# Kernel optimization log

Hardware: AMD Instinct MI355X
Metric: run time of the kernel (lower is better)

## Reference

```python
import jax, jax.numpy as jnp
import numpy as np
import math

D = 768
H = 12
DFF = 3072
HD = D // H


def _layernorm(x, g, b, eps=1e-5):
    mu = jnp.mean(x, axis=-1, keepdims=True)
    var = jnp.var(x, axis=-1, keepdims=True)
    return (x - mu) * jax.lax.rsqrt(var + eps) * g + b


def setup_inputs() -> dict:
    key = jax.random.key(0)
    ks = jax.random.split(key, 12)
    B, S = 2, 4096
    s = 1.0 / math.sqrt(D)
    sf = 1.0 / math.sqrt(DFF)
    return {
        "x": jax.random.normal(ks[0], (B, S, D), jnp.float32),
        "attention_mask": jnp.ones((B, S), jnp.int32),
        "ln1_g": jnp.ones((D,), jnp.float32),
        "ln1_b": jnp.zeros((D,), jnp.float32),
        "ln2_g": jnp.ones((D,), jnp.float32),
        "ln2_b": jnp.zeros((D,), jnp.float32),
        "Wq": jax.random.normal(ks[1], (D, D), jnp.float32) * s,
        "bq": jnp.zeros((D,), jnp.float32),
        "Wk": jax.random.normal(ks[2], (D, D), jnp.float32) * s,
        "bk": jnp.zeros((D,), jnp.float32),
        "Wv": jax.random.normal(ks[3], (D, D), jnp.float32) * s,
        "bv": jnp.zeros((D,), jnp.float32),
        "Wo": jax.random.normal(ks[4], (D, D), jnp.float32) * s,
        "bo": jnp.zeros((D,), jnp.float32),
        "W1": jax.random.normal(ks[5], (D, DFF), jnp.float32) * s,
        "b1": jnp.zeros((DFF,), jnp.float32),
        "W2": jax.random.normal(ks[6], (DFF, D), jnp.float32) * sf,
        "b2": jnp.zeros((D,), jnp.float32),
    }


def _block(x, attention_mask, ln1_g, ln1_b, ln2_g, ln2_b,
           Wq, bq, Wk, bk, Wv, bv, Wo, bo, W1, b1, W2, b2):
    B, S, _ = x.shape
    h = _layernorm(x, ln1_g, ln1_b)
    q = (h @ Wq + bq).reshape(B, S, H, HD)
    k = (h @ Wk + bk).reshape(B, S, H, HD)
    v = (h @ Wv + bv).reshape(B, S, H, HD)
    # scores: [B, H, S, S]
    dots = jnp.einsum('bqhd,bkhd->bhqk', q, k) / math.sqrt(HD)
    causal = jnp.tril(jnp.ones((S, S), bool))  # True = keep
    keep = causal[None, None] & (attention_mask != 0)[:, None, None, :]
    dots = jnp.where(keep, dots, -jnp.inf)
    probs = jax.nn.softmax(dots, axis=-1)
    ctx = jnp.einsum('bhqk,bkhd->bqhd', probs, v).reshape(B, S, D)
    sa = ctx @ Wo + bo  # dropout = identity (eval)
    x = x + sa
    h2 = _layernorm(x, ln2_g, ln2_b)
    ff = jax.nn.relu(h2 @ W1 + b1) @ W2 + b2
    return x + ff


def reference(x, attention_mask, ln1_g, ln1_b, ln2_g, ln2_b,
              Wq, bq, Wk, bk, Wv, bv, Wo, bo, W1, b1, W2, b2):
    return _block(x, attention_mask, ln1_g, ln1_b, ln2_g, ln2_b,
                  Wq, bq, Wk, bk, Wv, bv, Wo, bo, W1, b1, W2, b2)
```

## Files before the change

### kernel.cpp

```cpp
#include <hip/hip_runtime.h>
#include <hip/hip_bf16.h>
#include <math.h>

#define S_LEN 4096
#define DMODEL 768
#define NHEAD 12
#define HDIM 64
#define DFF_ 3072
#define MROWS 8192

typedef __bf16 bf16;
typedef __bf16 bf16x4 __attribute__((ext_vector_type(4)));
typedef __bf16 bf16x8 __attribute__((ext_vector_type(8)));
typedef float f32x4 __attribute__((ext_vector_type(4)));
typedef short s16x4 __attribute__((ext_vector_type(4)));

union F4 { float4 v; float f[4]; };
union U2 { bf16 h[2]; unsigned u; };
union U8 { unsigned u[4]; bf16x8 v; };

#if __has_builtin(__builtin_amdgcn_mfma_f32_16x16x16bf16_1k)
typedef s16x4 mf16_t;
#define MFMA16(a, b, c) __builtin_amdgcn_mfma_f32_16x16x16bf16_1k((a), (b), (c), 0, 0, 0)
#define HAVE_MFMA16 1
#elif __has_builtin(__builtin_amdgcn_mfma_f32_16x16x16_bf16)
typedef bf16x4 mf16_t;
#define MFMA16(a, b, c) __builtin_amdgcn_mfma_f32_16x16x16_bf16((a), (b), (c), 0, 0, 0)
#define HAVE_MFMA16 1
#else
#define HAVE_MFMA16 0
#endif

#if HAVE_MFMA16
union U4 { unsigned u[2]; mf16_t v; };
#endif

__device__ __forceinline__ void gld_lds16(void* lds, const void* g) {
    __builtin_amdgcn_global_load_lds(
        (const __attribute__((address_space(1))) unsigned int*)g,
        (__attribute__((address_space(3))) unsigned int*)lds, 16, 0, 0);
}

template<typename OUT>
__global__ __launch_bounds__(256) void ln_kernel(const float* __restrict__ x,
                                                 const float* __restrict__ g,
                                                 const float* __restrict__ bta,
                                                 OUT* __restrict__ out,
                                                 float* __restrict__ zb) {
    const int row = blockIdx.x;
    const int t = threadIdx.x;
    if (zb && row == 0 && t < 192)
        ((float4*)zb)[t] = make_float4(0.f, 0.f, 0.f, 0.f);
    const float* xr = x + (size_t)row * DMODEL;
    float v0 = xr[t], v1 = xr[t + 256], v2 = xr[t + 512];
    float s = v0 + v1 + v2;
    float ss = v0 * v0 + v1 * v1 + v2 * v2;
    for (int o = 32; o > 0; o >>= 1) {
        s += __shfl_down(s, o, 64);
        ss += __shfl_down(ss, o, 64);
    }
    __shared__ float sm[4], sm2[4];
    const int w = t >> 6, lane = t & 63;
    if (lane == 0) { sm[w] = s; sm2[w] = ss; }
    __syncthreads();
    s = sm[0] + sm[1] + sm[2] + sm[3];
    ss = sm2[0] + sm2[1] + sm2[2] + sm2[3];
    const float mu = s * (1.0f / DMODEL);
    const float var = ss * (1.0f / DMODEL) - mu * mu;
    const float rs = rsqrtf(var + 1e-5f);
    OUT* orow = out + (size_t)row * DMODEL;
    orow[t]       = (OUT)((v0 - mu) * rs * g[t]       + bta[t]);
    orow[t + 256] = (OUT)((v1 - mu) * rs * g[t + 256] + bta[t + 256]);
    orow[t + 512] = (OUT)((v2 - mu) * rs * g[t + 512] + bta[t + 512]);
}

__global__ __launch_bounds__(256) void wtrans_all_kernel(
    const float* __restrict__ Wq, const float* __restrict__ Wk,
    const float* __restrict__ Wv, const float* __restrict__ Wo,
    const float* __restrict__ W1, const float* __restrict__ W2,
    bf16* __restrict__ Wqt, bf16* __restrict__ Wkt, bf16* __restrict__ Wvt,
    bf16* __restrict__ Wot, bf16* __restrict__ W1t, bf16* __restrict__ W2t) {
    int t = blockIdx.x;
    const float* W; bf16* Wt; int K, N;
    if      (t < 144)  { W = Wq; Wt = Wqt; K = 768;  N = 768;  }
    else if (t < 288)  { W = Wk; Wt = Wkt; K = 768;  N = 768;  t -= 144; }
    else if (t < 432)  { W = Wv; Wt = Wvt; K = 768;  N = 768;  t -= 288; }
    else if (t < 576)  { W = Wo; Wt = Wot; K = 768;  N = 768;  t -= 432; }
    else if (t < 1152) { W = W1; Wt = W1t; K = 768;  N = 3072; t -= 576; }
    else               { W = W2; Wt = W2t; K = 3072; N = 768;  t -= 1152; }
    const int nx = N >> 6;
    const int n0 = (t % nx) * 64, k0 = (t / nx) * 64;

    __shared__ float tile[64][65];
    const int tid = threadIdx.x;
    const int lr = tid >> 4, lc = (tid & 15) << 2;
#pragma unroll
    for (int i = 0; i < 4; ++i) {
        const int r = lr + i * 16;
        F4 w; w.v = *(const float4*)&W[(size_t)(k0 + r) * N + n0 + lc];
#pragma unroll
        for (int j = 0; j < 4; ++j) tile[r][lc + j] = w.f[j];
    }
    __syncthreads();
#pragma unroll
    for (int i = 0; i < 4; ++i) {
        const int n = lr + i * 16;
        bf16x4 o;
#pragma unroll
        for (int j = 0; j < 4; ++j) o[j] = (bf16)tile[lc + j][n];
        *(bf16x4*)&Wt[(size_t)(n0 + n) * K + k0 + lc] = o;
    }
}

template<int MT, bool RELU, bool RES, bool OUT_BF16>
__global__ __launch_bounds__(256) void mgemm_kernel(
    const bf16* __restrict__ A,
    const bf16* __restrict__ Wt0, const float* __restrict__ bias0, void* __restrict__ C0,
    const bf16* __restrict__ Wt1, const float* __restrict__ bias1, void* __restrict__ C1,
    const bf16* __restrict__ Wt2, const float* __restrict__ bias2, void* __restrict__ C2,
    const float* __restrict__ R, int M, int N, int K, int Kloop,
    int koff0, int koff1, int koff2,
    float sc0, float sc1, float sc2) {
    const bf16* Wt = Wt0; const float* bias = bias0; void* C = C0; float sc = sc0; int koff = koff0;
    if (blockIdx.z == 1) { Wt = Wt1; bias = bias1; C = C1; sc = sc1; koff = koff1; }
    if (blockIdx.z == 2) { Wt = Wt2; bias = bias2; C = C2; sc = sc2; koff = koff2; }

    const int gx = gridDim.x;
    const int nwg = gx * gridDim.y;
    const int chunk = nwg >> 3;
    int lid = blockIdx.y * gx + blockIdx.x;
    lid = (lid & 7) * chunk + (lid >> 3);
    const int row0 = (lid / gx) * MT, col0 = (lid % gx) * 128;

    constexpr int NI = (MT == 128) ? 4 : 2;
    __shared__ bf16 As[2][MT * 32];
    __shared__ bf16 Bs[2][128 * 32];

    const int tid = threadIdx.x;
    const int wave = tid >> 6, lane = tid & 63;
    const int wr = (MT == 128) ? (wave >> 1) * 64 : 0;
    const int wc = (MT == 128) ? (wave & 1) * 64 : wave * 32;
    const int mrow = lane & 15, kq = (lane >> 4) * 8;

    const int st_row = (lane >> 2);
    const int st_off = (lane & 3) * 16;

    f32x4 acc[4][NI] = {};

    const char* Ab = (const char*)(A + (size_t)row0 * K + koff);
    const char* Bb = (const char*)(Wt + (size_t)col0 * K + koff);
    const size_t strideA = (size_t)K * 2;

    for (int k0 = 0; k0 < Kloop; k0 += 64) {
#pragma unroll
        for (int s = 0; s < 2; ++s) {
            const int kk = k0 + s * 32;
            if (MT == 128) {
#pragma unroll
                for (int issue = 0; issue < 2; ++issue) {
                    const int r = wave * 32 + issue * 16 + st_row;
                    gld_lds16((char*)As[s] + (wave * 32 + issue * 16) * 64,
                              Ab + (size_t)r * strideA + kk * 2 + st_off);
                }
            } else {
                const int r = wave * 16 + st_row;
                gld_lds16((char*)As[s] + (wave * 16) * 64,
                          Ab + (size_t)r * strideA + kk * 2 + st_off);
            }
#pragma unroll
            for (int issue = 0; issue < 2; ++issue) {
                const int r = wave * 32 + issue * 16 + st_row;
                gld_lds16((char*)Bs[s] + (wave * 32 + issue * 16) * 64,
                          Bb + (size_t)r * strideA + kk * 2 + st_off);
            }
        }
        __syncthreads();
#pragma unroll
        for (int s = 0; s < 2; ++s) {
            bf16x8 af[4], bfr[NI];
#pragma unroll
            for (int mi = 0; mi < 4; ++mi)
                af[mi] = *(const bf16x8*)&As[s][(wr + mi * 16 + mrow) * 32 + kq];
#pragma unroll
            for (int ni = 0; ni < NI; ++ni)
                bfr[ni] = *(const bf16x8*)&Bs[s][(wc + ni * 16 + mrow) * 32 + kq];
#pragma unroll
            for (int mi = 0; mi < 4; ++mi)
#pragma unroll
                for (int ni = 0; ni < NI; ++ni)
                    acc[mi][ni] = __builtin_amdgcn_mfma_f32_16x16x32_bf16(
                        bfr[ni], af[mi], acc[mi][ni], 0, 0, 0);
        }
        __syncthreads();
    }

    const int quad = lane >> 4;
#pragma unroll
    for (int ni = 0; ni < NI; ++ni) {
        const int col = col0 + wc + ni * 16 + quad * 4;
        F4 bv4; bv4.v = *(const float4*)&bias[col];
#pragma unroll
        for (int mi = 0; mi < 4; ++mi) {
            const int row = row0 + wr + mi * 16 + mrow;
            F4 o;
#pragma unroll
            for (int r = 0; r < 4; ++r) o.f[r] = acc[mi][ni][r] + bv4.f[r];
            if (RES) {
                F4 rr; rr.v = *(const float4*)&R[(size_t)row * N + col];
#pragma unroll
                for (int r = 0; r < 4; ++r) o.f[r] += rr.f[r];
            }
#pragma unroll
            for (int r = 0; r < 4; ++r) {
                o.f[r] *= sc;
                if (RELU) o.f[r] = fmaxf(o.f[r], 0.0f);
            }
            if (OUT_BF16) {
                bf16x4 ob;
#pragma unroll
                for (int r = 0; r < 4; ++r) ob[r] = (bf16)o.f[r];
                *(bf16x4*)&((bf16*)C)[(size_t)row * N + col] = ob;
            } else {
                *(float4*)&((float*)C)[(size_t)row * N + col] = o.v;
            }
        }
    }
}

__global__ __launch_bounds__(256) void mattn_kernel(
    const bf16* __restrict__ Q, const bf16* __restrict__ K,
    const bf16* __restrict__ V, const int* __restrict__ amask,
    bf16* __restrict__ O) {
    const int bx = blockIdx.x, h = blockIdx.y, b = blockIdx.z;

    __shared__ bf16 Ks[2][64][68];
#if HAVE_MFMA16
    __shared__ bf16 Vt[2][80][68];
#else
    __shared__ bf16 Vt[2][64][68];
#endif
    __shared__ bf16 Os[64][68];
    __shared__ float mk[2][64];
    __shared__ int flagv[2];

    const int tid = threadIdx.x;
    const int wave = tid >> 6, lane = tid & 63;
    const int l = lane & 15, quad = lane >> 4;
#if !HAVE_MFMA16
    const int qh = quad >> 1;
    const int srcA = (quad & 1) * 32 + l;
    const int srcB = srcA + 16;
#endif
    const float NEG_INF = -__builtin_huge_valf();

    const int kr = tid >> 2, ks = (tid & 3) * 16;
    const int vk0 = (tid & 31) * 2, vds = (tid >> 5) * 8;

    const bf16* Kbase = K + (size_t)b * S_LEN * DMODEL + h * HDIM;
    const bf16* Vbase = V + (size_t)b * S_LEN * DMODEL + h * HDIM;

#if HAVE_MFMA16
    if (tid < 68) {
        Vt[0][64][tid] = (bf16)1.0f;
        Vt[1][64][tid] = (bf16)1.0f;
    }
#endif

#pragma unroll 1
    for (int pass = 0; pass < 2; ++pass) {
        const int qt = pass ? bx : (63 - bx);

        const bf16* Qb = Q + (size_t)(b * S_LEN + qt * 64 + wave * 16 + l) * DMODEL + h * HDIM;
        const bf16x8 qf0 = *(const bf16x8*)(Qb + quad * 8);
        const bf16x8 qf1 = *(const bf16x8*)(Qb + 32 + quad * 8);

        float m_run = NEG_INF;
#if !HAVE_MFMA16
        float l_run = 0.0f;
#endif
        f32x4 acc[4] = {};
#if HAVE_MFMA16
        f32x4 acc_l = {};
#endif

        bf16x8 kp0, kp1, vp0, vp1;
        int mv = 1;
        {
            const bf16* kg = Kbase + (size_t)kr * DMODEL + ks;
            kp0 = *(const bf16x8*)kg;
            kp1 = *(const bf16x8*)(kg + 8);
            const bf16* vg = Vbase + (size_t)vk0 * DMODEL + vds;
            vp0 = *(const bf16x8*)vg;
            vp1 = *(const bf16x8*)(vg + DMODEL);
            if (wave == 0) mv = amask[b * S_LEN + lane];
        }
        __syncthreads();
        {
            *(bf16x8*)&Ks[0][kr][ks]     = kp0;
            *(bf16x8*)&Ks[0][kr][ks + 8] = kp1;
#pragma unroll
            for (int i = 0; i < 8; ++i) {
                U2 w; w.h[0] = vp0[i]; w.h[1] = vp1[i];
                *(unsigned*)&Vt[0][vds + i][vk0] = w.u;
            }
            if (wave == 0) {
                mk[0][lane] = mv ? 0.0f : NEG_INF;
                unsigned long long bal = __ballot(mv != 0);
                if (lane == 0) flagv[0] = (bal == ~0ULL);
            }
        }
        __syncthreads();
        int buf = 0;

        for (int kt = 0; kt <= qt; ++kt) {
            const bool more = (kt < qt);
            if (more) {
                const bf16* kg = Kbase + (size_t)((kt + 1) * 64 + kr) * DMODEL + ks;
                kp0 = *(const bf16x8*)kg;
                kp1 = *(const bf16x8*)(kg + 8);
                const bf16* vg = Vbase + (size_t)((kt + 1) * 64 + vk0) * DMODEL + vds;
                vp0 = *(const bf16x8*)vg;
                vp1 = *(const bf16x8*)(vg + DMODEL);
                if (wave == 0) mv = amask[b * S_LEN + (kt + 1) * 64 + lane];
            }

            const int allv = flagv[buf];
            f32x4 sreg[4] = {};
            __builtin_amdgcn_s_setprio(1);
#pragma unroll
            for (int mi = 0; mi < 4; ++mi) {
                bf16x8 kf0 = *(const bf16x8*)&Ks[buf][mi * 16 + l][quad * 8];
                bf16x8 kf1 = *(const bf16x8*)&Ks[buf][mi * 16 + l][32 + quad * 8];
                sreg[mi] = __builtin_amdgcn_mfma_f32_16x16x32_bf16(kf0, qf0, sreg[mi], 0, 0, 0);
                sreg[mi] = __builtin_amdgcn_mfma_f32_16x16x32_bf16(kf1, qf1, sreg[mi], 0, 0, 0);
            }
            __builtin_amdgcn_s_setprio(0);
            if (!allv) {
#pragma unroll
                for (int mi = 0; mi < 4; ++mi) {
                    F4 m4; m4.v = *(const float4*)&mk[buf][mi * 16 + quad * 4];
#pragma unroll
                    for (int r = 0; r < 4; ++r) sreg[mi][r] += m4.f[r];
                }
            }
            if (kt == qt) {
#pragma unroll
                for (int mi = 0; mi < 4; ++mi)
#pragma unroll
                    for (int r = 0; r < 4; ++r)
                        if (mi * 16 + quad * 4 + r > wave * 16 + l)
                            sreg[mi][r] = NEG_INF;
            }

            float mloc = sreg[0][0];
#pragma unroll
            for (int mi = 0; mi < 4; ++mi)
#pragma unroll
                for (int r = 0; r < 4; ++r) mloc = fmaxf(mloc, sreg[mi][r]);
            mloc = fmaxf(mloc, __shfl_xor(mloc, 16, 64));
            mloc = fmaxf(mloc, __shfl_xor(mloc, 32, 64));
            if (__any(mloc > m_run + 8.0f)) {
                const float mn = fmaxf(m_run, mloc);
                const float alpha = __builtin_amdgcn_exp2f(m_run - mn);
                m_run = mn;
#pragma unroll
                for (int mi = 0; mi < 4; ++mi)
#pragma unroll
                    for (int r = 0; r < 4; ++r) acc[mi][r] *= alpha;
#if HAVE_MFMA16
#pragma unroll
                for (int r = 0; r < 4; ++r) acc_l[r] *= alpha;
#else
                l_run *= alpha;
#endif
            }
#pragma unroll
            for (int mi = 0; mi < 4; ++mi)
#pragma unroll
                for (int r = 0; r < 4; ++r)
                    sreg[mi][r] = __builtin_amdgcn_exp2f(sreg[mi][r] - m_run);
#if !HAVE_MFMA16
            float ls = 0.0f;
#pragma unroll
            for (int mi = 0; mi < 4; ++mi)
#pragma unroll
                for (int r = 0; r < 4; ++r) ls += sreg[mi][r];
            ls += __shfl_xor(ls, 16, 64);
            ls += __shfl_xor(ls, 32, 64);
            l_run += ls;
#endif

            unsigned pk[4][2];
#pragma unroll
            for (int mi = 0; mi < 4; ++mi) {
                U2 w0; w0.h[0] = (bf16)sreg[mi][0]; w0.h[1] = (bf16)sreg[mi][1];
                U2 w1; w1.h[0] = (bf16)sreg[mi][2]; w1.h[1] = (bf16)sreg[mi][3];
                pk[mi][0] = w0.u; pk[mi][1] = w1.u;
            }

#if HAVE_MFMA16
            __builtin_amdgcn_s_setprio(1);
#pragma unroll
            for (int mi = 0; mi < 4; ++mi) {
                U4 pb; pb.u[0] = pk[mi][0]; pb.u[1] = pk[mi][1];
#pragma unroll
                for (int di = 0; di < 4; ++di) {
                    mf16_t va = *(const mf16_t*)&Vt[buf][di * 16 + l][mi * 16 + quad * 4];
                    acc[di] = MFMA16(va, pb.v, acc[di]);
                }
                mf16_t vl = *(const mf16_t*)&Vt[buf][64 + l][mi * 16 + quad * 4];
                acc_l = MFMA16(vl, pb.v, acc_l);
            }
            __builtin_amdgcn_s_setprio(0);
#else
            bf16x8 pfrag[2];
#pragma unroll
            for (int kc = 0; kc < 2; ++kc) {
                U8 u;
#pragma unroll
                for (int t = 0; t < 2; ++t) {
                    const unsigned a0 = (unsigned)__shfl((int)pk[2 * kc][t],     srcA, 64);
                    const unsigned b0 = (unsigned)__shfl((int)pk[2 * kc + 1][t], srcA, 64);
                    u.u[t] = qh ? b0 : a0;
                    const unsigned a1 = (unsigned)__shfl((int)pk[2 * kc][t],     srcB, 64);
                    const unsigned b1 = (unsigned)__shfl((int)pk[2 * kc + 1][t], srcB, 64);
                    u.u[2 + t] = qh ? b1 : a1;
                }
                pfrag[kc] = u.v;
            }
#pragma unroll
            for (int mi = 0; mi < 4; ++mi) {
                bf16x8 vf0 = *(const bf16x8*)&Vt[buf][mi * 16 + l][quad * 8];
                bf16x8 vf1 = *(const bf16x8*)&Vt[buf][mi * 16 + l][32 + quad * 8];
                acc[mi] = __builtin_amdgcn_mfma_f32_16x16x32_bf16(vf0, pfrag[0], acc[mi], 0, 0, 0);
                acc[mi] = __builtin_amdgcn_mfma_f32_16x16x32_bf16(vf1, pfrag[1], acc[mi], 0, 0, 0);
            }
#endif

            if (more) {
                const int nb = buf ^ 1;
                *(bf16x8*)&Ks[nb][kr][ks]     = kp0;
                *(bf16x8*)&Ks[nb][kr][ks + 8] = kp1;
#pragma unroll
                for (int i = 0; i < 8; ++i) {
                    U2 w; w.h[0] = vp0[i]; w.h[1] = vp1[i];
                    *(unsigned*)&Vt[nb][vds + i][vk0] = w.u;
                }
                if (wave == 0) {
                    mk[nb][lane] = mv ? 0.0f : NEG_INF;
                    unsigned long long bal = __ballot(mv != 0);
                    if (lane == 0) flagv[nb] = (bal == ~0ULL);
                }
            }
            __syncthreads();
            buf ^= 1;
        }

#if HAVE_MFMA16
        const float l_run = __shfl(acc_l[0], l, 64);
#endif
        const float rinv = 1.0f / l_run;
#pragma unroll
        for (int mi = 0; mi < 4; ++mi) {
            U2 w0; w0.h[0] = (bf16)(acc[mi][0] * rinv); w0.h[1] = (bf16)(acc[mi][1] * rinv);
            U2 w1; w1.h[0] = (bf16)(acc[mi][2] * rinv); w1.h[1] = (bf16)(acc[mi][3] * rinv);
            *(unsigned*)&Os[wave * 16 + l][mi * 16 + quad * 4]     = w0.u;
            *(unsigned*)&Os[wave * 16 + l][mi * 16 + quad * 4 + 2] = w1.u;
        }
        __syncthreads();
        {
            const int orow = tid >> 2, oseg = (tid & 3) * 16;
            bf16* Og = O + (size_t)(b * S_LEN + qt * 64 + orow) * DMODEL + h * HDIM + oseg;
            *(bf16x8*)Og       = *(const bf16x8*)&Os[orow][oseg];
            *(bf16x8*)(Og + 8) = *(const bf16x8*)&Os[orow][oseg + 8];
        }
    }
}

extern "C" void kernel_launch(void* const* d_in, const int* in_sizes, int n_in,
                              void* d_out, int out_size, void* d_ws, size_t ws_size,
                              hipStream_t stream) {
    const float* x     = (const float*)d_in[0];
    const int*   amask = (const int*)  d_in[1];
    const float* ln1_g = (const float*)d_in[2];
    const float* ln1_b = (const float*)d_in[3];
    const float* ln2_g = (const float*)d_in[4];
    const float* ln2_b = (const float*)d_in[5];
    const float* Wq = (const float*)d_in[6];  const float* bq = (const float*)d_in[7];
    const float* Wk = (const float*)d_in[8];  const float* bk = (const float*)d_in[9];
    const float* Wv = (const float*)d_in[10]; const float* bv = (const float*)d_in[11];
    const float* Wo = (const float*)d_in[12]; const float* bo = (const float*)d_in[13];
    const float* W1 = (const float*)d_in[14]; const float* b1 = (const float*)d_in[15];
    const float* W2 = (const float*)d_in[16]; const float* b2 = (const float*)d_in[17];
    float* out = (float*)d_out;

    char* ws = (char*)d_ws;
    const size_t WSML = (size_t)DMODEL * DMODEL * 2;
    const size_t WBIG = (size_t)DMODEL * DFF_ * 2;
    bf16* Wqt = (bf16*)(ws + 0 * WSML);
    bf16* Wkt = (bf16*)(ws + 1 * WSML);
    bf16* Wvt = (bf16*)(ws + 2 * WSML);
    bf16* Wot = (bf16*)(ws + 3 * WSML);
    bf16* W1t = (bf16*)(ws + 4 * WSML);
    bf16* W2t = (bf16*)(ws + 4 * WSML + WBIG);
    char* act = ws + 4 * WSML + 2 * WBIG;

    const size_t HB = (size_t)MROWS * DMODEL * 2;
    const size_t FB = (size_t)MROWS * DMODEL * 4;
    bf16*  h    = (bf16*)(act);
    bf16*  qb   = (bf16*)(act + HB);
    bf16*  kb   = (bf16*)(act + 2 * HB);
    bf16*  vb   = (bf16*)(act + 3 * HB);
    bf16*  ctx  = h;
    float* x1   = (float*)(act + 4 * HB);
    bf16*  f    = (bf16*)(act + 4 * HB + FB);
    bf16*  h2   = h;

    const float SCL = 0.125f * 1.44269504089f;

    wtrans_all_kernel<<<1728, 256, 0, stream>>>(Wq, Wk, Wv, Wo, W1, W2,
                                                Wqt, Wkt, Wvt, Wot, W1t, W2t);

    ln_kernel<bf16><<<MROWS, 256, 0, stream>>>(x, ln1_g, ln1_b, h, nullptr);
    mgemm_kernel<128, false, false, true><<<dim3(DMODEL / 128, MROWS / 128, 3), 256, 0, stream>>>(
        h, Wqt, bq, qb, Wkt, bk, kb, Wvt, bv, vb, nullptr,
        MROWS, DMODEL, DMODEL, DMODEL, 0, 0, 0, SCL, 1.0f, 1.0f);
    mattn_kernel<<<dim3(32, NHEAD, 2), 256, 0, stream>>>(qb, kb, vb, amask, ctx);
    mgemm_kernel<64, false, true, false><<<dim3(DMODEL / 128, MROWS / 64, 1), 256, 0, stream>>>(
        ctx, Wot, bo, x1, Wot, bo, x1, Wot, bo, x1, x,
        MROWS, DMODEL, DMODEL, DMODEL, 0, 0, 0, 1.0f, 1.0f, 1.0f);
    ln_kernel<bf16><<<MROWS, 256, 0, stream>>>(x1, ln2_g, ln2_b, h2, nullptr);
    mgemm_kernel<128, true, false, true><<<dim3(DFF_ / 128, MROWS / 128, 1), 256, 0, stream>>>(
        h2, W1t, b1, f, W1t, b1, f, W1t, b1, f, nullptr,
        MROWS, DFF_, DMODEL, DMODEL, 0, 0, 0, 1.0f, 1.0f, 1.0f);
    mgemm_kernel<64, false, true, false><<<dim3(DMODEL / 128, MROWS / 64, 1), 256, 0, stream>>>(
        f, W2t, b2, out, W2t, b2, out, W2t, b2, out, x1,
        MROWS, DMODEL, DFF_, DFF_, 0, 0, 0, 1.0f, 1.0f, 1.0f);
}
```

Baseline: 451.3 us.

## Pre-transpose V and stream K/V tiles into swizzled LDS via direct global loads

Adds a separate kernel that transposes V per head into a [d][seq] layout. The attention kernel then loads K and V^T tiles straight into LDS with global_load_lds, using an XOR swizzle in place of register staging, padded arrays and in-register V transposes. The row-sum MFMA now uses a constant ones fragment instead of an extra ones row in LDS. The intent is to cut VGPR pressure, LDS store work and bank conflicts in the attention loop, at the cost of one extra kernel launch and a pass over V through global memory.

```diff
diff --git a/kernel.cpp b/kernel.cpp
--- a/kernel.cpp
+++ b/kernel.cpp
@@ -14,31 +14,29 @@
 typedef __bf16 bf16x8 __attribute__((ext_vector_type(8)));
 typedef float f32x4 __attribute__((ext_vector_type(4)));
 typedef short s16x4 __attribute__((ext_vector_type(4)));
+typedef s16x4 frag4;
 
 union F4 { float4 v; float f[4]; };
 union U2 { bf16 h[2]; unsigned u; };
-union U8 { unsigned u[4]; bf16x8 v; };
-
-#if __has_builtin(__builtin_amdgcn_mfma_f32_16x16x16bf16_1k)
-typedef s16x4 mf16_t;
-#define MFMA16(a, b, c) __builtin_amdgcn_mfma_f32_16x16x16bf16_1k((a), (b), (c), 0, 0, 0)
-#define HAVE_MFMA16 1
-#elif __has_builtin(__builtin_amdgcn_mfma_f32_16x16x16_bf16)
-typedef bf16x4 mf16_t;
-#define MFMA16(a, b, c) __builtin_amdgcn_mfma_f32_16x16x16_bf16((a), (b), (c), 0, 0, 0)
-#define HAVE_MFMA16 1
-#else
-#define HAVE_MFMA16 0
-#endif
-
-#if HAVE_MFMA16
-union U4 { unsigned u[2]; mf16_t v; };
-#endif
+union P4 { unsigned u[2]; frag4 v; };
 
 __device__ __forceinline__ void gld_lds16(void* lds, const void* g) {
     __builtin_amdgcn_global_load_lds(
         (const __attribute__((address_space(1))) unsigned int*)g,
         (__attribute__((address_space(3))) unsigned int*)lds, 16, 0, 0);
+}
+
+__device__ __forceinline__ f32x4 mfma16(frag4 a, frag4 b, f32x4 c) {
+#if __has_builtin(__builtin_amdgcn_mfma_f32_16x16x16bf16_1k)
+    return __builtin_amdgcn_mfma_f32_16x16x16bf16_1k(a, b, c, 0, 0, 0);
+#else
+    union { frag4 s; bf16x4 h; } ua, ub; ua.s = a; ub.s = b;
+    bf16x8 a8 = {ua.h[0], ua.h[1], ua.h[2], ua.h[3],
+                 (bf16)0.f, (bf16)0.f, (bf16)0.f, (bf16)0.f};
+    bf16x8 b8 = {ub.h[0], ub.h[1], ub.h[2], ub.h[3],
+                 (bf16)0.f, (bf16)0.f, (bf16)0.f, (bf16)0.f};
+    return __builtin_amdgcn_mfma_f32_16x16x32_bf16(a8, b8, c, 0, 0, 0);
+#endif
 }
 
 template<typename OUT>
@@ -112,6 +110,28 @@
     }
 }
 
+__global__ __launch_bounds__(256) void vtrans_kernel(const bf16* __restrict__ vb,
+                                                     bf16* __restrict__ vbt) {
+    const int kt = blockIdx.x, h = blockIdx.y, b = blockIdx.z;
+    __shared__ bf16 tile[64][65];
+    const int t = threadIdx.x;
+    const int kl = t >> 2, ds = (t & 3) * 16;
+    const bf16* src = vb + (size_t)(b * S_LEN + kt * 64 + kl) * DMODEL + h * HDIM + ds;
+    *(bf16x8*)&tile[kl][ds]     = *(const bf16x8*)src;
+    *(bf16x8*)&tile[kl][ds + 8] = *(const bf16x8*)(src + 8);
+    __syncthreads();
+    const int d = t >> 2;
+    bf16* drow = vbt + (size_t)((b * NHEAD + h) * HDIM + d) * S_LEN + kt * 64;
+#pragma unroll
+    for (int c = 0; c < 2; ++c) {
+        const int k0 = (t & 3) * 16 + c * 8;
+        bf16x8 o;
+#pragma unroll
+        for (int j = 0; j < 8; ++j) o[j] = tile[k0 + j][d];
+        *(bf16x8*)(drow + k0) = o;
+    }
+}
+
 template<int MT, bool RELU, bool RES, bool OUT_BF16>
 __global__ __launch_bounds__(256) void mgemm_kernel(
     const bf16* __restrict__ A,
@@ -229,16 +249,12 @@
 
 __global__ __launch_bounds__(256) void mattn_kernel(
     const bf16* __restrict__ Q, const bf16* __restrict__ K,
-    const bf16* __restrict__ V, const int* __restrict__ amask,
+    const bf16* __restrict__ Vt, const int* __restrict__ amask,
     bf16* __restrict__ O) {
     const int bx = blockIdx.x, h = blockIdx.y, b = blockIdx.z;
 
-    __shared__ bf16 Ks[2][64][68];
-#if HAVE_MFMA16
-    __shared__ bf16 Vt[2][80][68];
-#else
-    __shared__ bf16 Vt[2][64][68];
-#endif
+    __shared__ bf16 Ks[2][4096];
+    __shared__ bf16 Vs[2][4096];
     __shared__ bf16 Os[64][68];
     __shared__ float mk[2][64];
     __shared__ int flagv[2];
@@ -246,25 +262,25 @@
     const int tid = threadIdx.x;
     const int wave = tid >> 6, lane = tid & 63;
     const int l = lane & 15, quad = lane >> 4;
-#if !HAVE_MFMA16
-    const int qh = quad >> 1;
-    const int srcA = (quad & 1) * 32 + l;
-    const int srcB = srcA + 16;
-#endif
     const float NEG_INF = -__builtin_huge_valf();
 
-    const int kr = tid >> 2, ks = (tid & 3) * 16;
-    const int vk0 = (tid & 31) * 2, vds = (tid >> 5) * 8;
+    const int g1 = 256 + tid;
+    const int rw0 = tid >> 3, pc0 = tid & 7;
+    const int rw1 = g1 >> 3,  pc1 = g1 & 7;
+    const int koff0 = rw0 * DMODEL + ((pc0 ^ (rw0 & 7)) << 3);
+    const int koff1 = rw1 * DMODEL + ((pc1 ^ (rw1 & 7)) << 3);
+    const int voff0 = rw0 * S_LEN + ((pc0 ^ (rw0 & 7)) << 3);
+    const int voff1 = rw1 * S_LEN + ((pc1 ^ (rw1 & 7)) << 3);
 
     const bf16* Kbase = K + (size_t)b * S_LEN * DMODEL + h * HDIM;
-    const bf16* Vbase = V + (size_t)b * S_LEN * DMODEL + h * HDIM;
-
-#if HAVE_MFMA16
-    if (tid < 68) {
-        Vt[0][64][tid] = (bf16)1.0f;
-        Vt[1][64][tid] = (bf16)1.0f;
-    }
-#endif
+    const bf16* Vtb = Vt + (size_t)((b * NHEAD + h) * HDIM) * S_LEN;
+
+    const int sw = (l & 7) << 4;
+    const int krd0 = l * 128 + ((quad << 4) ^ sw);
+    const int krd1 = l * 128 + (((4 + quad) << 4) ^ sw);
+
+    P4 onesu; onesu.u[0] = 0x3F803F80u; onesu.u[1] = 0x3F803F80u;
+    const frag4 onesA = onesu.v;
 
 #pragma unroll 1
     for (int pass = 0; pass < 2; ++pass) {
@@ -275,62 +291,51 @@
         const bf16x8 qf1 = *(const bf16x8*)(Qb + 32 + quad * 8);
 
         float m_run = NEG_INF;
-#if !HAVE_MFMA16
-        float l_run = 0.0f;
-#endif
         f32x4 acc[4] = {};
-#if HAVE_MFMA16
         f32x4 acc_l = {};
-#endif
-
-        bf16x8 kp0, kp1, vp0, vp1;
-        int mv = 1;
+
         {
-            const bf16* kg = Kbase + (size_t)kr * DMODEL + ks;
-            kp0 = *(const bf16x8*)kg;
-            kp1 = *(const bf16x8*)(kg + 8);
-            const bf16* vg = Vbase + (size_t)vk0 * DMODEL + vds;
-            vp0 = *(const bf16x8*)vg;
-            vp1 = *(const bf16x8*)(vg + DMODEL);
-            if (wave == 0) mv = amask[b * S_LEN + lane];
-        }
-        __syncthreads();
-        {
-            *(bf16x8*)&Ks[0][kr][ks]     = kp0;
-            *(bf16x8*)&Ks[0][kr][ks + 8] = kp1;
-#pragma unroll
-            for (int i = 0; i < 8; ++i) {
-                U2 w; w.h[0] = vp0[i]; w.h[1] = vp1[i];
-                *(unsigned*)&Vt[0][vds + i][vk0] = w.u;
-            }
+            char* kd = (char*)Ks[0] + wave * 1024;
+            char* vd = (char*)Vs[0] + wave * 1024;
+            gld_lds16(kd,        Kbase + koff0);
+            gld_lds16(kd + 4096, Kbase + koff1);
+            gld_lds16(vd,        Vtb + voff0);
+            gld_lds16(vd + 4096, Vtb + voff1);
             if (wave == 0) {
-                mk[0][lane] = mv ? 0.0f : NEG_INF;
-                unsigned long long bal = __ballot(mv != 0);
+                int mv0 = amask[b * S_LEN + lane];
+                mk[0][lane] = mv0 ? 0.0f : NEG_INF;
+                unsigned long long bal = __ballot(mv0 != 0);
                 if (lane == 0) flagv[0] = (bal == ~0ULL);
             }
         }
         __syncthreads();
         int buf = 0;
+        int mv = 1;
 
         for (int kt = 0; kt <= qt; ++kt) {
             const bool more = (kt < qt);
             if (more) {
-                const bf16* kg = Kbase + (size_t)((kt + 1) * 64 + kr) * DMODEL + ks;
-                kp0 = *(const bf16x8*)kg;
-                kp1 = *(const bf16x8*)(kg + 8);
-                const bf16* vg = Vbase + (size_t)((kt + 1) * 64 + vk0) * DMODEL + vds;
-                vp0 = *(const bf16x8*)vg;
-                vp1 = *(const bf16x8*)(vg + DMODEL);
+                const bf16* kg = Kbase + (size_t)(kt + 1) * 64 * DMODEL;
+                const bf16* vg = Vtb + (kt + 1) * 64;
+                const int nb = buf ^ 1;
+                char* kd = (char*)Ks[nb] + wave * 1024;
+                char* vd = (char*)Vs[nb] + wave * 1024;
+                gld_lds16(kd,        kg + koff0);
+                gld_lds16(kd + 4096, kg + koff1);
+                gld_lds16(vd,        vg + voff0);
+                gld_lds16(vd + 4096, vg + voff1);
                 if (wave == 0) mv = amask[b * S_LEN + (kt + 1) * 64 + lane];
             }
 
             const int allv = flagv[buf];
+            const char* Ksb = (const char*)Ks[buf];
+            const char* Vsb = (const char*)Vs[buf];
             f32x4 sreg[4] = {};
             __builtin_amdgcn_s_setprio(1);
 #pragma unroll
             for (int mi = 0; mi < 4; ++mi) {
-                bf16x8 kf0 = *(const bf16x8*)&Ks[buf][mi * 16 + l][quad * 8];
-                bf16x8 kf1 = *(const bf16x8*)&Ks[buf][mi * 16 + l][32 + quad * 8];
+                bf16x8 kf0 = *(const bf16x8*)(Ksb + mi * 2048 + krd0);
+                bf16x8 kf1 = *(const bf16x8*)(Ksb + mi * 2048 + krd1);
                 sreg[mi] = __builtin_amdgcn_mfma_f32_16x16x32_bf16(kf0, qf0, sreg[mi], 0, 0, 0);
                 sreg[mi] = __builtin_amdgcn_mfma_f32_16x16x32_bf16(kf1, qf1, sreg[mi], 0, 0, 0);
             }
@@ -364,31 +369,17 @@
                 const float alpha = __builtin_amdgcn_exp2f(m_run - mn);
                 m_run = mn;
 #pragma unroll
-                for (int mi = 0; mi < 4; ++mi)
-#pragma unroll
-                    for (int r = 0; r < 4; ++r) acc[mi][r] *= alpha;
-#if HAVE_MFMA16
+                for (int di = 0; di < 4; ++di)
+#pragma unroll
+                    for (int r = 0; r < 4; ++r) acc[di][r] *= alpha;
 #pragma unroll
                 for (int r = 0; r < 4; ++r) acc_l[r] *= alpha;
-#else
-                l_run *= alpha;
-#endif
             }
 #pragma unroll
             for (int mi = 0; mi < 4; ++mi)
 #pragma unroll
                 for (int r = 0; r < 4; ++r)
                     sreg[mi][r] = __builtin_amdgcn_exp2f(sreg[mi][r] - m_run);
-#if !HAVE_MFMA16
-            float ls = 0.0f;
-#pragma unroll
-            for (int mi = 0; mi < 4; ++mi)
-#pragma unroll
-                for (int r = 0; r < 4; ++r) ls += sreg[mi][r];
-            ls += __shfl_xor(ls, 16, 64);
-            ls += __shfl_xor(ls, 32, 64);
-            l_run += ls;
-#endif
 
             unsigned pk[4][2];
 #pragma unroll
@@ -398,68 +389,32 @@
                 pk[mi][0] = w0.u; pk[mi][1] = w1.u;
             }
 
-#if HAVE_MFMA16
             __builtin_amdgcn_s_setprio(1);
 #pragma unroll
             for (int mi = 0; mi < 4; ++mi) {
-                U4 pb; pb.u[0] = pk[mi][0]; pb.u[1] = pk[mi][1];
+                P4 pb; pb.u[0] = pk[mi][0]; pb.u[1] = pk[mi][1];
+                const int vb_mi = (((mi << 5) | (quad << 3)) ^ sw);
 #pragma unroll
                 for (int di = 0; di < 4; ++di) {
-                    mf16_t va = *(const mf16_t*)&Vt[buf][di * 16 + l][mi * 16 + quad * 4];
-                    acc[di] = MFMA16(va, pb.v, acc[di]);
+                    frag4 va = *(const frag4*)(Vsb + di * 2048 + l * 128 + vb_mi);
+                    acc[di] = mfma16(va, pb.v, acc[di]);
                 }
-                mf16_t vl = *(const mf16_t*)&Vt[buf][64 + l][mi * 16 + quad * 4];
-                acc_l = MFMA16(vl, pb.v, acc_l);
+                acc_l = mfma16(onesA, pb.v, acc_l);
             }
             __builtin_amdgcn_s_setprio(0);
-#else
-            bf16x8 pfrag[2];
-#pragma unroll
-            for (int kc = 0; kc < 2; ++kc) {
-                U8 u;
-#pragma unroll
-                for (int t = 0; t < 2; ++t) {
-                    const unsigned a0 = (unsigned)__shfl((int)pk[2 * kc][t],     srcA, 64);
-                    const unsigned b0 = (unsigned)__shfl((int)pk[2 * kc + 1][t], srcA, 64);
-                    u.u[t] = qh ? b0 : a0;
-                    const unsigned a1 = (unsigned)__shfl((int)pk[2 * kc][t],     srcB, 64);
-                    const unsigned b1 = (unsigned)__shfl((int)pk[2 * kc + 1][t], srcB, 64);
-                    u.u[2 + t] = qh ? b1 : a1;
-                }
-                pfrag[kc] = u.v;
-            }
-#pragma unroll
-            for (int mi = 0; mi < 4; ++mi) {
-                bf16x8 vf0 = *(const bf16x8*)&Vt[buf][mi * 16 + l][quad * 8];
-                bf16x8 vf1 = *(const bf16x8*)&Vt[buf][mi * 16 + l][32 + quad * 8];
-                acc[mi] = __builtin_amdgcn_mfma_f32_16x16x32_bf16(vf0, pfrag[0], acc[mi], 0, 0, 0);
-                acc[mi] = __builtin_amdgcn_mfma_f32_16x16x32_bf16(vf1, pfrag[1], acc[mi], 0, 0, 0);
-            }
-#endif
-
-            if (more) {
+
+            if (more && wave == 0) {
                 const int nb = buf ^ 1;
-                *(bf16x8*)&Ks[nb][kr][ks]     = kp0;
-                *(bf16x8*)&Ks[nb][kr][ks + 8] = kp1;
-#pragma unroll
-                for (int i = 0; i < 8; ++i) {
-                    U2 w; w.h[0] = vp0[i]; w.h[1] = vp1[i];
-                    *(unsigned*)&Vt[nb][vds + i][vk0] = w.u;
-                }
-                if (wave == 0) {
-                    mk[nb][lane] = mv ? 0.0f : NEG_INF;
-                    unsigned long long bal = __ballot(mv != 0);
-                    if (lane == 0) flagv[nb] = (bal == ~0ULL);
-                }
+                mk[nb][lane] = mv ? 0.0f : NEG_INF;
+                unsigned long long bal = __ballot(mv != 0);
+                if (lane == 0) flagv[nb] = (bal == ~0ULL);
             }
             __syncthreads();
             buf ^= 1;
         }
 
-#if HAVE_MFMA16
-        const float l_run = __shfl(acc_l[0], l, 64);
-#endif
-        const float rinv = 1.0f / l_run;
+        const float l_fin = __shfl(acc_l[0], l, 64);
+        const float rinv = 1.0f / l_fin;
 #pragma unroll
         for (int mi = 0; mi < 4; ++mi) {
             U2 w0; w0.h[0] = (bf16)(acc[mi][0] * rinv); w0.h[1] = (bf16)(acc[mi][1] * rinv);
@@ -474,6 +429,7 @@
             *(bf16x8*)Og       = *(const bf16x8*)&Os[orow][oseg];
             *(bf16x8*)(Og + 8) = *(const bf16x8*)&Os[orow][oseg + 8];
         }
+        __syncthreads();
     }
 }
 
@@ -515,6 +471,7 @@
     float* x1   = (float*)(act + 4 * HB);
     bf16*  f    = (bf16*)(act + 4 * HB + FB);
     bf16*  h2   = h;
+    bf16*  vbt  = f;
 
     const float SCL = 0.125f * 1.44269504089f;
 
@@ -525,7 +482,8 @@
     mgemm_kernel<128, false, false, true><<<dim3(DMODEL / 128, MROWS / 128, 3), 256, 0, stream>>>(
         h, Wqt, bq, qb, Wkt, bk, kb, Wvt, bv, vb, nullptr,
         MROWS, DMODEL, DMODEL, DMODEL, 0, 0, 0, SCL, 1.0f, 1.0f);
-    mattn_kernel<<<dim3(32, NHEAD, 2), 256, 0, stream>>>(qb, kb, vb, amask, ctx);
+    vtrans_kernel<<<dim3(S_LEN / 64, NHEAD, 2), 256, 0, stream>>>(vb, vbt);
+    mattn_kernel<<<dim3(32, NHEAD, 2), 256, 0, stream>>>(qb, kb, vbt, amask, ctx);
     mgemm_kernel<64, false, true, false><<<dim3(DMODEL / 128, MROWS / 64, 1), 256, 0, stream>>>(
         ctx, Wot, bo, x1, Wot, bo, x1, Wot, bo, x1, x,
         MROWS, DMODEL, DMODEL, DMODEL, 0, 0, 0, 1.0f, 1.0f, 1.0f);
```

Result: no change. 450.4 us (-0.2%).
